# Performance work log

Hardware: AMD Instinct MI355X
Metric: run time of the kernel (lower is better)

The kernel has to match this reference:

```python
import jax, jax.numpy as jnp
import numpy as np

N_ACTORS = 50000
N_EDGES = 800000
D = 128
L = 2
EDGE_IN = 2 * D + 2  # src feat + rel (x,y) + dst feat


def setup_inputs() -> dict:
    key = jax.random.key(0)
    ks = jax.random.split(key, 6)
    actor_features = jax.random.normal(ks[0], (N_ACTORS, D), dtype=jnp.float32)
    edge_dist_rel = jax.random.normal(ks[1], (N_EDGES, 2), dtype=jnp.float32)
    # per-layer learned weights (bias=False in both Linears)
    W_att = jax.random.normal(ks[2], (L, EDGE_IN), dtype=jnp.float32) * 0.05
    W_emb = jax.random.normal(ks[3], (L, D, EDGE_IN), dtype=jnp.float32) * 0.05
    edge_src_idx = jax.random.randint(ks[4], (N_EDGES,), 0, N_ACTORS, dtype=jnp.int32)
    edge_dst_idx = jax.random.randint(ks[5], (N_EDGES,), 0, N_ACTORS, dtype=jnp.int32)
    return {
        "actor_features": actor_features,
        "edge_dist_rel": edge_dist_rel,
        "W_att": W_att,
        "W_emb": W_emb,
        "edge_src_idx": edge_src_idx,
        "edge_dst_idx": edge_dst_idx,
    }


def _scatter_softmax(scores, dst_idx, num_segments):
    # numerically stable softmax over irregular dst groups
    seg_max = jax.ops.segment_max(scores, dst_idx, num_segments=num_segments)
    ex = jnp.exp(scores - seg_max[dst_idx])
    denom = jax.ops.segment_sum(ex, dst_idx, num_segments=num_segments)
    return ex / denom[dst_idx]


def reference(actor_features, edge_dist_rel, W_att, W_emb, edge_src_idx, edge_dst_idx):
    n = actor_features.shape[0]
    feat = actor_features
    for l in range(W_att.shape[0]):  # small fixed number of layers
        # gather per-edge features and build edge inputs [E, 2D+2]
        e_in = jnp.concatenate(
            [feat[edge_src_idx], edge_dist_rel, feat[edge_dst_idx]], axis=-1)
        # edge attention: Linear(edge_in -> 1, no bias) + LeakyReLU(0.2)
        s = jax.nn.leaky_relu(e_in @ W_att[l], negative_slope=0.2)  # [E]
        att = _scatter_softmax(s, edge_dst_idx, n)  # dropout omitted (eval mode)
        # edge embed: Linear(edge_in -> D, no bias)
        emb = e_in @ W_emb[l].T  # [E, D]
        agg = jax.ops.segment_sum(att[:, None] * emb, edge_dst_idx, num_segments=n)
        feat = jax.nn.relu(agg)
    return feat
```

## Files before the change

### kernel.cpp

```cpp
#include <hip/hip_runtime.h>
#include <hip/hip_fp16.h>

#define D 128
#define EDGE_IN 258

typedef __attribute__((ext_vector_type(8))) short bf16x8;
typedef __attribute__((ext_vector_type(4))) float f32x4;

__device__ __forceinline__ float rl_f(float v, int j) {
  return __int_as_float(__builtin_amdgcn_readlane(__float_as_int(v), j));
}
__device__ __forceinline__ int rl_i(int v, int j) {
  return __builtin_amdgcn_readlane(v, j);
}
__device__ __forceinline__ ushort f32_to_bf16(float f) {
  unsigned u = __float_as_uint(f);
  unsigned r = (u + 0x7FFFu + ((u >> 16) & 1u)) >> 16;
  return (ushort)r;
}
__device__ __forceinline__ float bf16_to_f32(ushort h) {
  return __uint_as_float(((unsigned)h) << 16);
}

__global__ void zero_int(int* __restrict__ p, int n) {
  int i = blockIdx.x * blockDim.x + threadIdx.x;
  if (i < n) p[i] = 0;
}

__global__ void hist_kernel(const int* __restrict__ dst, int* __restrict__ deg, int ne) {
  int base = blockIdx.x * 1024 + threadIdx.x;
#pragma unroll
  for (int k = 0; k < 4; k++) {
    int e = base + k * 256;
    if (e < ne) atomicAdd(&deg[dst[e]], 1);
  }
}

__global__ __launch_bounds__(256) void scan_part(const int* __restrict__ deg,
                                                 int* __restrict__ bsum, int n) {
  __shared__ int red[256];
  int b = blockIdx.x, tid = threadIdx.x;
  int base = b * 1024 + tid * 4;
  int s = 0;
#pragma unroll
  for (int j = 0; j < 4; j++) { int idx = base + j; if (idx < n) s += deg[idx]; }
  red[tid] = s;
  __syncthreads();
  for (int off = 128; off; off >>= 1) {
    if (tid < off) red[tid] += red[tid + off];
    __syncthreads();
  }
  if (tid == 0) bsum[b] = red[0];
}

__global__ __launch_bounds__(256) void scan_bsums(int* __restrict__ bsum, int nb) {
  __shared__ int part[256];
  int tid = threadIdx.x;
  int v = (tid < nb) ? bsum[tid] : 0;
  part[tid] = v;
  __syncthreads();
  for (int off = 1; off < 256; off <<= 1) {
    int t = (tid >= off) ? part[tid - off] : 0;
    __syncthreads();
    part[tid] += t;
    __syncthreads();
  }
  if (tid < nb) bsum[tid] = (tid == 0) ? 0 : part[tid - 1];
}

__global__ __launch_bounds__(256) void scan_final(const int* __restrict__ deg,
                                                  const int* __restrict__ bsumex,
                                                  int* __restrict__ offs,
                                                  int* __restrict__ cur, int n, int ne) {
  __shared__ int part[256];
  int b = blockIdx.x, tid = threadIdx.x;
  int base = b * 1024 + tid * 4;
  int v[4];
  int s = 0;
#pragma unroll
  for (int j = 0; j < 4; j++) {
    int idx = base + j;
    v[j] = (idx < n) ? deg[idx] : 0;
    s += v[j];
  }
  part[tid] = s;
  __syncthreads();
  for (int off = 1; off < 256; off <<= 1) {
    int t = (tid >= off) ? part[tid - off] : 0;
    __syncthreads();
    part[tid] += t;
    __syncthreads();
  }
  int run = bsumex[b] + ((tid == 0) ? 0 : part[tid - 1]);
#pragma unroll
  for (int j = 0; j < 4; j++) {
    int idx = base + j;
    if (idx < n) { offs[idx] = run; cur[idx] = run; run += v[j]; }
  }
  if (b == 0 && tid == 0) offs[n] = ne;
}

__global__ void scatter_kernel(const int* __restrict__ dst, const int* __restrict__ srcIdx,
                               const float2* __restrict__ rel, int* __restrict__ cur,
                               int2* __restrict__ meta, int ne) {
  int base = blockIdx.x * 1024 + threadIdx.x;
  int e[4], p[4];
  int2 mv[4];
  int cnt = 0;
#pragma unroll
  for (int k = 0; k < 4; k++) {
    int ek = base + k * 256;
    if (ek < ne) {
      float2 r = rel[ek];
      __half2 h = __floats2half2_rn(r.x, r.y);
      mv[cnt].x = srcIdx[ek];
      mv[cnt].y = *(int*)&h;
      e[cnt] = ek;
      cnt++;
    }
  }
#pragma unroll
  for (int k = 0; k < 4; k++)
    if (k < cnt) p[k] = atomicAdd(&cur[dst[e[k]]], 1);
#pragma unroll
  for (int k = 0; k < 4; k++)
    if (k < cnt) meta[p[k]] = mv[k];
}

__global__ void prep_weights(const float* __restrict__ W_emb,
                             const float* __restrict__ W_att,
                             ushort* __restrict__ WBhi, ushort* __restrict__ WBlo) {
  int lane = threadIdx.x;
  int kt = blockIdx.x / 9, nt = blockIdx.x % 9;
  int part = blockIdx.y, l = blockIdx.z;
  int off = part ? 130 : 0;
  int g = lane >> 4, nn = lane & 15;
  int n = nt * 16 + nn;
  size_t base = (((size_t)((l * 2 + part) * 4 + kt) * 9 + nt) * 64 + lane) * 8;
#pragma unroll
  for (int e = 0; e < 8; e++) {
    int k = kt * 32 + 8 * g + e;
    float val = 0.f;
    if (nt < 8) val = W_emb[(size_t)(l * D + n) * EDGE_IN + off + k];
    else if (nn == 0) val = W_att[(size_t)l * EDGE_IN + off + k];
    ushort hi = f32_to_bf16(val);
    WBhi[base + e] = hi;
    WBlo[base + e] = f32_to_bf16(val - bf16_to_f32(hi));
  }
}

__global__ void rel_prep(const float* __restrict__ W_emb, float* __restrict__ Wrel) {
  int d = threadIdx.x;
  int c = blockIdx.x;
  int l = blockIdx.y;
  Wrel[(l * 2 + c) * 128 + d] = W_emb[(size_t)(l * D + d) * EDGE_IN + 128 + c];
}

__global__ __launch_bounds__(128) void proj_kernel(
    const float* __restrict__ feat, const ushort* __restrict__ WBhi,
    const ushort* __restrict__ WBlo, __half* __restrict__ Ps16,
    float* __restrict__ Pd, float* __restrict__ a_s, float* __restrict__ a_d,
    int n, int l) {
  __shared__ ushort Ahi[4][64][8];
  __shared__ ushort Alo[4][64][8];
  int i0 = blockIdx.x * 16;
  int tid = threadIdx.x;

  for (int t = tid; t < 512; t += 128) {
    int m = t >> 5;
    int k4 = t & 31;
    int gi = i0 + m;
    float4 v = (gi < n) ? ((const float4*)feat)[(size_t)gi * 32 + k4]
                        : make_float4(0.f, 0.f, 0.f, 0.f);
    int kt = k4 >> 3;
    int lanew = m + 16 * ((k4 >> 1) & 3);
    int eh = (k4 & 1) * 4;
    ushort hx = f32_to_bf16(v.x), hy = f32_to_bf16(v.y);
    ushort hz = f32_to_bf16(v.z), hw = f32_to_bf16(v.w);
    ushort4 h4 = make_ushort4(hx, hy, hz, hw);
    ushort4 l4 = make_ushort4(f32_to_bf16(v.x - bf16_to_f32(hx)),
                              f32_to_bf16(v.y - bf16_to_f32(hy)),
                              f32_to_bf16(v.z - bf16_to_f32(hz)),
                              f32_to_bf16(v.w - bf16_to_f32(hw)));
    *(ushort4*)&Ahi[kt][lanew][eh] = h4;
    *(ushort4*)&Alo[kt][lanew][eh] = l4;
  }
  __syncthreads();

  int w = tid >> 6;
  int lane = tid & 63;

  bf16x8 ah[4], al[4];
#pragma unroll
  for (int kt = 0; kt < 4; kt++) {
    ah[kt] = *(const bf16x8*)&Ahi[kt][lane][0];
    al[kt] = *(const bf16x8*)&Alo[kt][lane][0];
  }

  const ushort* bh = WBhi + (size_t)(l * 2 + w) * 4 * 9 * 64 * 8;
  const ushort* bl = WBlo + (size_t)(l * 2 + w) * 4 * 9 * 64 * 8;

  f32x4 acc[9];
#pragma unroll
  for (int i = 0; i < 9; i++) acc[i] = (f32x4){0.f, 0.f, 0.f, 0.f};

#pragma unroll
  for (int nt = 0; nt < 9; nt++) {
#pragma unroll
    for (int kt = 0; kt < 4; kt++) {
      size_t idx = (((size_t)kt * 9 + nt) * 64 + lane) * 8;
      bf16x8 bhv = *(const bf16x8*)&bh[idx];
      bf16x8 blv = *(const bf16x8*)&bl[idx];
      acc[nt] = __builtin_amdgcn_mfma_f32_16x16x32_bf16(ah[kt], bhv, acc[nt], 0, 0, 0);
      acc[nt] = __builtin_amdgcn_mfma_f32_16x16x32_bf16(al[kt], bhv, acc[nt], 0, 0, 0);
      acc[nt] = __builtin_amdgcn_mfma_f32_16x16x32_bf16(ah[kt], blv, acc[nt], 0, 0, 0);
    }
  }

  int col0 = lane & 15, rowg = lane >> 4;
  if (w == 0) {
#pragma unroll
    for (int nt = 0; nt < 8; nt++)
#pragma unroll
      for (int r = 0; r < 4; r++) {
        int gi = i0 + rowg * 4 + r;
        if (gi < n) Ps16[(size_t)gi * D + nt * 16 + col0] = __float2half(acc[nt][r]);
      }
    if (col0 == 0) {
#pragma unroll
      for (int r = 0; r < 4; r++) {
        int gi = i0 + rowg * 4 + r;
        if (gi < n) a_s[gi] = acc[8][r];
      }
    }
  } else {
#pragma unroll
    for (int nt = 0; nt < 8; nt++)
#pragma unroll
      for (int r = 0; r < 4; r++) {
        int gi = i0 + rowg * 4 + r;
        if (gi < n) Pd[(size_t)gi * D + nt * 16 + col0] = acc[nt][r];
      }
    if (col0 == 0) {
#pragma unroll
      for (int r = 0; r < 4; r++) {
        int gi = i0 + rowg * 4 + r;
        if (gi < n) a_d[gi] = acc[8][r];
      }
    }
  }
}

__global__ __launch_bounds__(256) void edge_kernel(
    const __half2* __restrict__ Ps, const float* __restrict__ Pd,
    const float* __restrict__ a_s, const float* __restrict__ a_d,
    const int2* __restrict__ meta, const int* __restrict__ offs,
    const float* __restrict__ Wrel, const float* __restrict__ W_att,
    float* __restrict__ out, int n, int l) {
  int wid = (blockIdx.x * blockDim.x + threadIdx.x) >> 6;
  if (wid >= n) return;
  int lane = threadIdx.x & 63;
  int d0 = 2 * lane;
  float wax = W_att[(size_t)l * EDGE_IN + 128];
  float way = W_att[(size_t)l * EDGE_IN + 129];
  float ad = a_d[wid];
  int p0 = offs[wid], p1 = offs[wid + 1];
  float m = -1e30f, lsum = 0.f, Sx = 0.f, Sy = 0.f;
  float accx = 0.f, accy = 0.f;
  for (int c0 = p0; c0 < p1; c0 += 64) {
    int cn = min(64, p1 - c0);
    int si = 0;
    float rx = 0.f, ry = 0.f, s = -1e30f;
    if (lane < cn) {
      int2 mt = meta[c0 + lane];
      si = mt.x;
      float2 rr = __half22float2(*(__half2*)&mt.y);
      rx = rr.x;
      ry = rr.y;
      float sc = a_s[si] + ad + rx * wax + ry * way;
      s = (sc > 0.f) ? sc : 0.2f * sc;
    }
    float cm = s;
#pragma unroll
    for (int o = 32; o; o >>= 1) cm = fmaxf(cm, __shfl_xor(cm, o, 64));
    float mnew = fmaxf(m, cm);
    float corr = __expf(m - mnew);
    float w = (lane < cn) ? __expf(s - mnew) : 0.f;
    float cw = w, cwx = w * rx, cwy = w * ry;
#pragma unroll
    for (int o = 32; o; o >>= 1) {
      cw += __shfl_xor(cw, o, 64);
      cwx += __shfl_xor(cwx, o, 64);
      cwy += __shfl_xor(cwy, o, 64);
    }
    lsum = lsum * corr + cw;
    Sx = Sx * corr + cwx;
    Sy = Sy * corr + cwy;
    accx *= corr;
    accy *= corr;
    m = mnew;
    int j = 0;
    for (; j + 8 <= cn; j += 8) {
      float2 f[8];
      float wj[8];
#pragma unroll
      for (int q = 0; q < 8; q++) {
        int sj = rl_i(si, j + q);
        wj[q] = rl_f(w, j + q);
        f[q] = __half22float2(Ps[(size_t)sj * 64 + lane]);
      }
#pragma unroll
      for (int q = 0; q < 8; q++) {
        accx += wj[q] * f[q].x;
        accy += wj[q] * f[q].y;
      }
    }
    if (j < cn) {
      float2 f[8];
      float wj[8];
      int r = cn - j;
#pragma unroll
      for (int q = 0; q < 8; q++) {
        if (q < r) {
          int sj = rl_i(si, j + q);
          wj[q] = rl_f(w, j + q);
          f[q] = __half22float2(Ps[(size_t)sj * 64 + lane]);
        }
      }
#pragma unroll
      for (int q = 0; q < 8; q++) {
        if (q < r) {
          accx += wj[q] * f[q].x;
          accy += wj[q] * f[q].y;
        }
      }
    }
  }
  float2 o2 = make_float2(0.f, 0.f);
  if (p1 > p0) {
    const float2 wc0 = *(const float2*)&Wrel[(l * 2 + 0) * 128 + d0];
    const float2 wc1 = *(const float2*)&Wrel[(l * 2 + 1) * 128 + d0];
    float inv = 1.0f / lsum;
    float2 pd = *(const float2*)&Pd[(size_t)wid * D + d0];
    accx += Sx * wc0.x + Sy * wc1.x;
    accy += Sx * wc0.y + Sy * wc1.y;
    o2.x = fmaxf(accx * inv + pd.x, 0.f);
    o2.y = fmaxf(accy * inv + pd.y, 0.f);
  }
  *(float2*)&out[(size_t)wid * D + d0] = o2;
}

extern "C" void kernel_launch(void* const* d_in, const int* in_sizes, int n_in,
                              void* d_out, int out_size, void* d_ws, size_t ws_size,
                              hipStream_t stream) {
  const float* actor = (const float*)d_in[0];
  const float* rel   = (const float*)d_in[1];
  const float* W_att = (const float*)d_in[2];
  const float* W_emb = (const float*)d_in[3];
  const int* srcIdx  = (const int*)d_in[4];
  const int* dstIdx  = (const int*)d_in[5];
  int n  = in_sizes[0] / D;
  int ne = in_sizes[4];
  int Lnum = in_sizes[2] / EDGE_IN;
  float* fout_last = (float*)d_out;

  float* ws = (float*)d_ws;
  size_t o = 0;
  int2* meta = (int2*)ws; o += 2 * (size_t)ne;
  size_t wbN = (size_t)Lnum * 2 * 4 * 9 * 64 * 8;
  ushort* WBhi = (ushort*)(ws + o); o += (wbN + 1) / 2;
  ushort* WBlo = (ushort*)(ws + o); o += (wbN + 1) / 2;
  float* Wre = ws + o; o += (size_t)Lnum * 2 * 128;
  float* Pd  = ws + o; o += (size_t)n * D;
  float* a_s = ws + o; o += (size_t)n + 64;
  float* a_d = ws + o; o += (size_t)n + 64;
  __half* Ps16 = (__half*)(ws + o); o += (size_t)n * D / 2;
  int* ibuf = (int*)(ws + o);
  size_t io = 0;
  int* deg  = ibuf + io; io += n + 64;
  int* offs = ibuf + io; io += n + 64;
  int* cur  = ibuf + io; io += n + 64;
  int* bsum = ibuf + io; io += 256;

  int nb = (n + 1023) / 1024;
  int nbe = (ne + 1023) / 1024;

  zero_int<<<(n + 255) / 256, 256, 0, stream>>>(deg, n);
  hist_kernel<<<nbe, 256, 0, stream>>>(dstIdx, deg, ne);
  scan_part<<<nb, 256, 0, stream>>>(deg, bsum, n);
  scan_bsums<<<1, 256, 0, stream>>>(bsum, nb);
  scan_final<<<nb, 256, 0, stream>>>(deg, bsum, offs, cur, n, ne);
  scatter_kernel<<<nbe, 256, 0, stream>>>(dstIdx, srcIdx, (const float2*)rel, cur, meta, ne);
  prep_weights<<<dim3(36, 2, Lnum), 64, 0, stream>>>(W_emb, W_att, WBhi, WBlo);
  rel_prep<<<dim3(2, Lnum), 128, 0, stream>>>(W_emb, Wre);

  const float* fin = actor;
  int nt16 = (n + 15) / 16;
  for (int l = 0; l < Lnum; l++) {
    proj_kernel<<<nt16, 128, 0, stream>>>(fin, WBhi, WBlo, Ps16, Pd, a_s, a_d, n, l);
    edge_kernel<<<(n + 3) / 4, 256, 0, stream>>>((const __half2*)Ps16, Pd, a_s, a_d, meta,
                                                 offs, Wre, W_att, fout_last, n, l);
    fin = fout_last;
  }
}
```

Measured before the change: 350.5 us.

## Process four destination nodes per wave with 16-lane groups and wide loads

The edge aggregation kernel now gives each destination node a 16-lane group instead of a whole 64-lane wave, so one wave handles four nodes. Edges are taken in chunks of 16. Each lane accumulates 8 feature dimensions and reads them with one 16-byte load per edge, instead of 2 dimensions with a 4-byte load. Average in-degree is about 16, so the old 64-wide chunks left most lanes idle; this remap is meant to cut that waste and reduce the number of load instructions. The cost is divergence between the four groups when their degrees differ, and shuffle-based broadcasts that replace readlane.

```diff
diff --git a/kernel.cpp b/kernel.cpp
--- a/kernel.cpp
+++ b/kernel.cpp
@@ -7,12 +7,6 @@
 typedef __attribute__((ext_vector_type(8))) short bf16x8;
 typedef __attribute__((ext_vector_type(4))) float f32x4;
 
-__device__ __forceinline__ float rl_f(float v, int j) {
-  return __int_as_float(__builtin_amdgcn_readlane(__float_as_int(v), j));
-}
-__device__ __forceinline__ int rl_i(int v, int j) {
-  return __builtin_amdgcn_readlane(v, j);
-}
 __device__ __forceinline__ ushort f32_to_bf16(float f) {
   unsigned u = __float_as_uint(f);
   unsigned r = (u + 0x7FFFu + ((u >> 16) & 1u)) >> 16;
@@ -252,27 +246,34 @@
 }
 
 __global__ __launch_bounds__(256) void edge_kernel(
-    const __half2* __restrict__ Ps, const float* __restrict__ Pd,
+    const __half* __restrict__ Ps, const float* __restrict__ Pd,
     const float* __restrict__ a_s, const float* __restrict__ a_d,
     const int2* __restrict__ meta, const int* __restrict__ offs,
     const float* __restrict__ Wrel, const float* __restrict__ W_att,
     float* __restrict__ out, int n, int l) {
-  int wid = (blockIdx.x * blockDim.x + threadIdx.x) >> 6;
-  if (wid >= n) return;
+  int wave = (blockIdx.x * blockDim.x + threadIdx.x) >> 6;
   int lane = threadIdx.x & 63;
-  int d0 = 2 * lane;
+  int g = lane >> 4, lg = lane & 15;
+  int v = wave * 4 + g;
+  bool valid = v < n;
+  int p0 = 0, p1 = 0;
+  if (valid) { p0 = offs[v]; p1 = offs[v + 1]; }
   float wax = W_att[(size_t)l * EDGE_IN + 128];
   float way = W_att[(size_t)l * EDGE_IN + 129];
-  float ad = a_d[wid];
-  int p0 = offs[wid], p1 = offs[wid + 1];
+  float ad = valid ? a_d[v] : 0.f;
   float m = -1e30f, lsum = 0.f, Sx = 0.f, Sy = 0.f;
-  float accx = 0.f, accy = 0.f;
-  for (int c0 = p0; c0 < p1; c0 += 64) {
-    int cn = min(64, p1 - c0);
+  float acc[8];
+#pragma unroll
+  for (int i = 0; i < 8; i++) acc[i] = 0.f;
+  int gbase = g * 16;
+  int dbase = lg * 8;
+
+  for (int c0 = p0; c0 < p1; c0 += 16) {
+    int cn = min(16, p1 - c0);
     int si = 0;
     float rx = 0.f, ry = 0.f, s = -1e30f;
-    if (lane < cn) {
-      int2 mt = meta[c0 + lane];
+    if (lg < cn) {
+      int2 mt = meta[c0 + lg];
       si = mt.x;
       float2 rr = __half22float2(*(__half2*)&mt.y);
       rx = rr.x;
@@ -282,13 +283,13 @@
     }
     float cm = s;
 #pragma unroll
-    for (int o = 32; o; o >>= 1) cm = fmaxf(cm, __shfl_xor(cm, o, 64));
+    for (int o = 8; o; o >>= 1) cm = fmaxf(cm, __shfl_xor(cm, o, 64));
     float mnew = fmaxf(m, cm);
     float corr = __expf(m - mnew);
-    float w = (lane < cn) ? __expf(s - mnew) : 0.f;
+    float w = (lg < cn) ? __expf(s - mnew) : 0.f;
     float cw = w, cwx = w * rx, cwy = w * ry;
 #pragma unroll
-    for (int o = 32; o; o >>= 1) {
+    for (int o = 8; o; o >>= 1) {
       cw += __shfl_xor(cw, o, 64);
       cwx += __shfl_xor(cwx, o, 64);
       cwy += __shfl_xor(cwy, o, 64);
@@ -296,58 +297,62 @@
     lsum = lsum * corr + cw;
     Sx = Sx * corr + cwx;
     Sy = Sy * corr + cwy;
-    accx *= corr;
-    accy *= corr;
+#pragma unroll
+    for (int i = 0; i < 8; i++) acc[i] *= corr;
     m = mnew;
-    int j = 0;
-    for (; j + 8 <= cn; j += 8) {
-      float2 f[8];
-      float wj[8];
-#pragma unroll
-      for (int q = 0; q < 8; q++) {
-        int sj = rl_i(si, j + q);
-        wj[q] = rl_f(w, j + q);
-        f[q] = __half22float2(Ps[(size_t)sj * 64 + lane]);
-      }
-#pragma unroll
-      for (int q = 0; q < 8; q++) {
-        accx += wj[q] * f[q].x;
-        accy += wj[q] * f[q].y;
-      }
-    }
-    if (j < cn) {
-      float2 f[8];
-      float wj[8];
-      int r = cn - j;
-#pragma unroll
-      for (int q = 0; q < 8; q++) {
-        if (q < r) {
-          int sj = rl_i(si, j + q);
-          wj[q] = rl_f(w, j + q);
-          f[q] = __half22float2(Ps[(size_t)sj * 64 + lane]);
-        }
-      }
-#pragma unroll
-      for (int q = 0; q < 8; q++) {
-        if (q < r) {
-          accx += wj[q] * f[q].x;
-          accy += wj[q] * f[q].y;
-        }
-      }
-    }
-  }
-  float2 o2 = make_float2(0.f, 0.f);
-  if (p1 > p0) {
-    const float2 wc0 = *(const float2*)&Wrel[(l * 2 + 0) * 128 + d0];
-    const float2 wc1 = *(const float2*)&Wrel[(l * 2 + 1) * 128 + d0];
+
+    for (int j = 0; j < cn; j += 4) {
+      uint4 h[4];
+      float wj[4];
+#pragma unroll
+      for (int q = 0; q < 4; q++) {
+        int sj = __shfl(si, gbase + j + q, 64);
+        wj[q] = __shfl(w, gbase + j + q, 64);
+        h[q] = *(const uint4*)&Ps[(size_t)sj * D + dbase];
+      }
+#pragma unroll
+      for (int q = 0; q < 4; q++) {
+        float2 f0 = __half22float2(*(__half2*)&h[q].x);
+        float2 f1 = __half22float2(*(__half2*)&h[q].y);
+        float2 f2 = __half22float2(*(__half2*)&h[q].z);
+        float2 f3 = __half22float2(*(__half2*)&h[q].w);
+        acc[0] += wj[q] * f0.x;
+        acc[1] += wj[q] * f0.y;
+        acc[2] += wj[q] * f1.x;
+        acc[3] += wj[q] * f1.y;
+        acc[4] += wj[q] * f2.x;
+        acc[5] += wj[q] * f2.y;
+        acc[6] += wj[q] * f3.x;
+        acc[7] += wj[q] * f3.y;
+      }
+    }
+  }
+
+  float res[8];
+#pragma unroll
+  for (int i = 0; i < 8; i++) res[i] = 0.f;
+  if (valid && p1 > p0) {
     float inv = 1.0f / lsum;
-    float2 pd = *(const float2*)&Pd[(size_t)wid * D + d0];
-    accx += Sx * wc0.x + Sy * wc1.x;
-    accy += Sx * wc0.y + Sy * wc1.y;
-    o2.x = fmaxf(accx * inv + pd.x, 0.f);
-    o2.y = fmaxf(accy * inv + pd.y, 0.f);
-  }
-  *(float2*)&out[(size_t)wid * D + d0] = o2;
+    const float4* wc0p = (const float4*)&Wrel[(size_t)(l * 2 + 0) * 128 + dbase];
+    const float4* wc1p = (const float4*)&Wrel[(size_t)(l * 2 + 1) * 128 + dbase];
+    const float4* pdp = (const float4*)&Pd[(size_t)v * D + dbase];
+    float4 w0a = wc0p[0], w0b = wc0p[1];
+    float4 w1a = wc1p[0], w1b = wc1p[1];
+    float4 pda = pdp[0], pdb = pdp[1];
+    float c0v[8] = {w0a.x, w0a.y, w0a.z, w0a.w, w0b.x, w0b.y, w0b.z, w0b.w};
+    float c1v[8] = {w1a.x, w1a.y, w1a.z, w1a.w, w1b.x, w1b.y, w1b.z, w1b.w};
+    float pdv[8] = {pda.x, pda.y, pda.z, pda.w, pdb.x, pdb.y, pdb.z, pdb.w};
+#pragma unroll
+    for (int i = 0; i < 8; i++) {
+      float a = acc[i] + Sx * c0v[i] + Sy * c1v[i];
+      res[i] = fmaxf(a * inv + pdv[i], 0.f);
+    }
+  }
+  if (valid) {
+    float4* op = (float4*)&out[(size_t)v * D + dbase];
+    op[0] = make_float4(res[0], res[1], res[2], res[3]);
+    op[1] = make_float4(res[4], res[5], res[6], res[7]);
+  }
 }
 
 extern "C" void kernel_launch(void* const* d_in, const int* in_sizes, int n_in,
@@ -396,10 +401,11 @@
 
   const float* fin = actor;
   int nt16 = (n + 15) / 16;
+  int nbedge = (n + 15) / 16;
   for (int l = 0; l < Lnum; l++) {
     proj_kernel<<<nt16, 128, 0, stream>>>(fin, WBhi, WBlo, Ps16, Pd, a_s, a_d, n, l);
-    edge_kernel<<<(n + 3) / 4, 256, 0, stream>>>((const __half2*)Ps16, Pd, a_s, a_d, meta,
-                                                 offs, Wre, W_att, fout_last, n, l);
+    edge_kernel<<<nbedge, 256, 0, stream>>>(Ps16, Pd, a_s, a_d, meta,
+                                            offs, Wre, W_att, fout_last, n, l);
     fin = fout_last;
   }
 }
```

New measurement: 327.1 us. 1.07x faster.
